# Performance work log

Hardware: AMD Instinct MI355X
Metric: run time of the kernel (lower is better)

Reference implementation:

```python
import jax, jax.numpy as jnp
import numpy as np

N = 100000
IN_DIM = 512
HID = 256
C = 64  # output_dim / num_classes
E = 1_600_000


def setup_inputs() -> dict:
    key = jax.random.key(0)
    ks = jax.random.split(key, 8)
    x = jax.random.normal(ks[0], (N, IN_DIM), dtype=jnp.float32)
    edge_index = jax.random.randint(ks[1], (2, E), 0, N, dtype=jnp.int64)
    # learned params (Linear stores W as [out,in]; we use [in,out] and matmul)
    W1 = jax.random.normal(ks[2], (IN_DIM, HID), dtype=jnp.float32) / np.sqrt(IN_DIM)
    b1 = jnp.zeros((HID,), dtype=jnp.float32)
    W2 = jax.random.normal(ks[3], (HID, C), dtype=jnp.float32) / np.sqrt(HID)
    b2 = jnp.zeros((C,), dtype=jnp.float32)
    Wp = jax.random.normal(ks[4], (C, 1), dtype=jnp.float32) / np.sqrt(C)
    bp = jnp.zeros((1,), dtype=jnp.float32)
    return {"x": x, "edge_index": edge_index, "K": 10,
            "W1": W1, "b1": b1, "W2": W2, "b2": b2, "Wp": Wp, "bp": bp}


def reference(x, edge_index, K, W1, b1, W2, b2, Wp, bp):
    n = x.shape[0]
    # MLP encoder (dropout is identity in eval mode)
    h = jax.nn.relu(x @ W1 + b1)
    h = h @ W2 + b2  # [N, C]

    # gcn_norm with add_remaining_self_loops (fill_value=1.0):
    # original self-loop edges are dropped (weight 0), fresh self loops appended.
    row, col = edge_index[0], edge_index[1]
    ew = jnp.where(row == col, 0.0, 1.0).astype(h.dtype)
    loops = jnp.arange(n, dtype=edge_index.dtype)
    row_f = jnp.concatenate([row, loops])
    col_f = jnp.concatenate([col, loops])
    ew_f = jnp.concatenate([ew, jnp.ones((n,), dtype=h.dtype)])
    deg = jax.ops.segment_sum(ew_f, col_f, num_segments=n)
    dinv = jnp.where(deg > 0, jax.lax.rsqrt(deg), 0.0)
    norm = dinv[row_f] * ew_f * dinv[col_f]  # [E+N]

    # K hops of normalized scatter-add propagation
    def hop(hc, _):
        m = jax.ops.segment_sum(norm[:, None] * hc[row_f], col_f, num_segments=n)
        return m, m

    _, hs = jax.lax.scan(hop, h, None, length=K)  # hs: [K, N, C]
    pps = jnp.concatenate([h[:, None, :], jnp.moveaxis(hs, 0, 1)], axis=1)  # [N, K+1, C]

    # learned per-hop retain scores + combine
    score = jax.nn.sigmoid((pps @ Wp + bp)[..., 0])  # [N, K+1]
    emb = jnp.einsum('nk,nkc->nc', score, pps)  # [N, C]
    return jax.nn.log_softmax(emb, axis=1), emb
```

## Files before the change

kernel.cpp:

```cpp
#include <hip/hip_runtime.h>
#include <hip/hip_fp16.h>

typedef unsigned short u16;
typedef short bf16x8 __attribute__((ext_vector_type(8)));
typedef float f32x4 __attribute__((ext_vector_type(4)));

#define IN_DIM 512
#define HID    256
#define C_DIM  64
#define KHOPS  10
#define CHUNK  2048

__device__ inline u16 f2bf(float v) {
    unsigned u = __float_as_uint(v);
    return (u16)((u + 0x7FFFu + ((u >> 16) & 1u)) >> 16);
}

__device__ inline void unpack8(uint4 u, float* f) {
    float2 a = __half22float2(*(__half2*)&u.x);
    float2 b = __half22float2(*(__half2*)&u.y);
    float2 c = __half22float2(*(__half2*)&u.z);
    float2 d = __half22float2(*(__half2*)&u.w);
    f[0] = a.x; f[1] = a.y; f[2] = b.x; f[3] = b.y;
    f[4] = c.x; f[5] = c.y; f[6] = d.x; f[7] = d.y;
}

__global__ void k_deg(const int* __restrict__ ei, int E, unsigned* __restrict__ deg) {
    int e = blockIdx.x * blockDim.x + threadIdx.x;
    if (e >= E) return;
    int r = ei[e], c = ei[E + e];
    if (r != c) atomicAdd(&deg[c], 1u);
}

__global__ void k_dinv(const unsigned* __restrict__ deg, float* __restrict__ dinv, int n) {
    int v = blockIdx.x * blockDim.x + threadIdx.x;
    if (v >= n) return;
    dinv[v] = 1.0f / sqrtf((float)(deg[v] + 1u));
}

__global__ __launch_bounds__(256) void k_scanA(const unsigned* __restrict__ cnt, int n,
                                               unsigned* __restrict__ bsum) {
    __shared__ unsigned sd[256];
    int base = blockIdx.x * CHUNK;
    unsigned s = 0;
    for (int i = threadIdx.x; i < CHUNK; i += 256) {
        int idx = base + i;
        s += (idx < n) ? cnt[idx] : 0u;
    }
    sd[threadIdx.x] = s;
    __syncthreads();
    for (int ofs = 128; ofs > 0; ofs >>= 1) {
        if (threadIdx.x < ofs) sd[threadIdx.x] += sd[threadIdx.x + ofs];
        __syncthreads();
    }
    if (threadIdx.x == 0) bsum[blockIdx.x] = sd[0];
}

__global__ void k_scanB(unsigned* bsum, int nch, unsigned* rowptrN) {
    if (threadIdx.x == 0 && blockIdx.x == 0) {
        unsigned run = 0;
        for (int i = 0; i < nch; i++) { unsigned t = bsum[i]; bsum[i] = run; run += t; }
        *rowptrN = run;
    }
}

__global__ __launch_bounds__(256) void k_scanC(const unsigned* __restrict__ cnt, int n,
                                               const unsigned* __restrict__ bsum,
                                               unsigned* __restrict__ rowptr) {
    __shared__ unsigned sd[256];
    const int PT = CHUNK / 256;
    int base = blockIdx.x * CHUNK;
    unsigned c[PT];
    unsigned tot = 0;
#pragma unroll
    for (int j = 0; j < PT; j++) {
        int idx = base + threadIdx.x * PT + j;
        c[j] = (idx < n) ? cnt[idx] : 0u;
        tot += c[j];
    }
    sd[threadIdx.x] = tot;
    __syncthreads();
    for (int ofs = 1; ofs < 256; ofs <<= 1) {
        unsigned vv = (threadIdx.x >= (unsigned)ofs) ? sd[threadIdx.x - ofs] : 0u;
        __syncthreads();
        sd[threadIdx.x] += vv;
        __syncthreads();
    }
    unsigned excl = sd[threadIdx.x] - tot;
    unsigned run = bsum[blockIdx.x] + excl;
#pragma unroll
    for (int j = 0; j < PT; j++) {
        int idx = base + threadIdx.x * PT + j;
        if (idx < n) rowptr[idx] = run;
        run += c[j];
    }
}

__global__ void k_fill(const int* __restrict__ ei, int E, const unsigned* __restrict__ rowptr,
                       unsigned* __restrict__ fill, const float* __restrict__ dinv,
                       int2* __restrict__ epack) {
    int e = blockIdx.x * blockDim.x + threadIdx.x;
    if (e >= E) return;
    int r = ei[e], c = ei[E + e];
    if (r == c) return;
    unsigned pos = rowptr[c] + atomicAdd(&fill[c], 1u);
    int2 p;
    p.x = r;
    p.y = __float_as_int(dinv[r] * dinv[c]);
    epack[pos] = p;
}

__global__ void k_prepw(const float* __restrict__ W, u16* __restrict__ T, int K, int N) {
    int t = blockIdx.x * blockDim.x + threadIdx.x;
    if (t >= K * N) return;
    int k = t / N, nn = t - k * N;
    T[(size_t)nn * K + k] = f2bf(W[t]);
}

__global__ __launch_bounds__(256) void k_gemm1_mfma(
    const float* __restrict__ X, const u16* __restrict__ BT,
    const float* __restrict__ b1, u16* __restrict__ C, int M) {
    __shared__ uint4 smem4[2048];
    u16* Ab = (u16*)smem4;
    u16* Bb = Ab + 8192;
    const int tid = threadIdx.x, l = tid & 63, w = tid >> 6;
    const int wr = w >> 1, wc = w & 1;
    const int row0 = blockIdx.x * 128, col0 = blockIdx.y * 128;
    const int srow = tid >> 1, skh = tid & 1;
    const int rsw = (srow >> 1) & 3;
    const int m15 = l & 15;
    const int slotoff = (((l >> 4) ^ ((l >> 1) & 3)) << 3);

    f32x4 acc[4][4];
#pragma unroll
    for (int i = 0; i < 4; i++)
#pragma unroll
        for (int j = 0; j < 4; j++) acc[i][j] = (f32x4){0.f, 0.f, 0.f, 0.f};

    float ax[16];
    uint4 rb[2];
    auto gload = [&](int t) {
        int k0 = t * 32;
        int grow = row0 + srow;
        if (grow < M) {
            const float* p = X + (size_t)grow * IN_DIM + k0 + skh * 16;
#pragma unroll
            for (int q = 0; q < 4; q++) *(float4*)&ax[q * 4] = *(const float4*)(p + q * 4);
        } else {
#pragma unroll
            for (int q = 0; q < 16; q++) ax[q] = 0.f;
        }
        const u16* pb = BT + (size_t)(col0 + srow) * IN_DIM + k0 + skh * 16;
        rb[0] = *(const uint4*)pb;
        rb[1] = *(const uint4*)(pb + 8);
    };
    auto lwrite = [&](int buf) {
#pragma unroll
        for (int g = 0; g < 2; g++) {
            unsigned wd[4];
#pragma unroll
            for (int q = 0; q < 4; q++)
                wd[q] = (unsigned)f2bf(ax[g * 8 + 2 * q]) | ((unsigned)f2bf(ax[g * 8 + 2 * q + 1]) << 16);
            uint4 H = {wd[0], wd[1], wd[2], wd[3]};
            int slot = (skh * 2 + g) ^ rsw;
            *(uint4*)&Ab[buf * 4096 + srow * 32 + (slot << 3)] = H;
            *(uint4*)&Bb[buf * 4096 + srow * 32 + (slot << 3)] = rb[g];
        }
    };

    gload(0);
    lwrite(0);
    __syncthreads();
    const int NT = IN_DIM / 32;
    for (int t = 0; t < NT; t++) {
        int buf = t & 1;
        if (t + 1 < NT) gload(t + 1);
        bf16x8 af[4], bf[4];
#pragma unroll
        for (int f = 0; f < 4; f++) {
            af[f] = *(bf16x8*)&Ab[buf * 4096 + (wr * 64 + f * 16 + m15) * 32 + slotoff];
            bf[f] = *(bf16x8*)&Bb[buf * 4096 + (wc * 64 + f * 16 + m15) * 32 + slotoff];
        }
#pragma unroll
        for (int i = 0; i < 4; i++)
#pragma unroll
            for (int j = 0; j < 4; j++)
                acc[i][j] = __builtin_amdgcn_mfma_f32_16x16x32_bf16(af[i], bf[j], acc[i][j], 0, 0, 0);
        if (t + 1 < NT) {
            __syncthreads();
            lwrite((t + 1) & 1);
            __syncthreads();
        }
    }
    __syncthreads();
    u16* ot = (u16*)smem4;
#pragma unroll
    for (int j = 0; j < 4; j++) {
        int col = col0 + wc * 64 + j * 16 + m15;
        float bb = b1[col];
        int coll = wc * 64 + j * 16 + m15;
#pragma unroll
        for (int i = 0; i < 4; i++)
#pragma unroll
            for (int r = 0; r < 4; r++) {
                int rowl = wr * 64 + i * 16 + (l >> 4) * 4 + r;
                ot[rowl * 128 + coll] = f2bf(fmaxf(acc[i][j][r] + bb, 0.f));
            }
    }
    __syncthreads();
#pragma unroll
    for (int p = 0; p < 8; p++) {
        int idx = p * 4096 + tid * 16;
        uint4 vv = *(uint4*)((char*)smem4 + idx);
        int row = p * 16 + (tid >> 4);
        int gcol = (tid & 15) * 8;
        int grow = row0 + row;
        if (grow < M) *(uint4*)(C + (size_t)grow * HID + col0 + gcol) = vv;
    }
}

__global__ __launch_bounds__(256) void k_gemm2_mfma(
    const u16* __restrict__ A1, const u16* __restrict__ BT,
    const float* __restrict__ b2, __half* __restrict__ H, int M) {
    __shared__ u16 Ab[2][128][32], Bb[2][64][32];
    const int tid = threadIdx.x, l = tid & 63, w = tid >> 6;
    const int wr = w >> 1, wc = w & 1;
    const int row0 = blockIdx.x * 128;
    const int srow = tid >> 1, skh = tid & 1;
    const int rsw = (srow >> 1) & 3;
    const int srow2 = tid >> 2, skq = tid & 3;
    const int rsw2 = (srow2 >> 1) & 3;
    const int m15 = l & 15;
    const int slotoff = (((l >> 4) ^ ((l >> 1) & 3)) << 3);

    f32x4 acc[4][2];
#pragma unroll
    for (int i = 0; i < 4; i++)
#pragma unroll
        for (int j = 0; j < 2; j++) acc[i][j] = (f32x4){0.f, 0.f, 0.f, 0.f};

    uint4 ra[2], rb2;
    auto gload = [&](int t) {
        int k0 = t * 32;
        int grow = row0 + srow;
        if (grow < M) {
            const u16* p = A1 + (size_t)grow * HID + k0 + skh * 16;
            ra[0] = *(const uint4*)p;
            ra[1] = *(const uint4*)(p + 8);
        } else {
            ra[0] = ra[1] = (uint4){0u, 0u, 0u, 0u};
        }
        rb2 = *(const uint4*)(BT + (size_t)srow2 * HID + k0 + skq * 8);
    };
    auto lwrite = [&](int buf) {
#pragma unroll
        for (int g = 0; g < 2; g++) {
            int slot = (skh * 2 + g) ^ rsw;
            *(uint4*)&Ab[buf][srow][slot << 3] = ra[g];
        }
        int slot2 = skq ^ rsw2;
        *(uint4*)&Bb[buf][srow2][slot2 << 3] = rb2;
    };

    gload(0);
    lwrite(0);
    __syncthreads();
    const int NT = HID / 32;
    for (int t = 0; t < NT; t++) {
        int buf = t & 1;
        if (t + 1 < NT) gload(t + 1);
        bf16x8 af[4], bf[2];
#pragma unroll
        for (int f = 0; f < 4; f++)
            af[f] = *(bf16x8*)&Ab[buf][wr * 64 + f * 16 + m15][slotoff];
#pragma unroll
        for (int f = 0; f < 2; f++)
            bf[f] = *(bf16x8*)&Bb[buf][wc * 32 + f * 16 + m15][slotoff];
#pragma unroll
        for (int i = 0; i < 4; i++)
#pragma unroll
            for (int j = 0; j < 2; j++)
                acc[i][j] = __builtin_amdgcn_mfma_f32_16x16x32_bf16(af[i], bf[j], acc[i][j], 0, 0, 0);
        if (t + 1 < NT) {
            __syncthreads();
            lwrite((t + 1) & 1);
            __syncthreads();
        }
    }
#pragma unroll
    for (int j = 0; j < 2; j++) {
        int col = wc * 32 + j * 16 + m15;
        float bb = b2[col];
#pragma unroll
        for (int i = 0; i < 4; i++)
#pragma unroll
            for (int r = 0; r < 4; r++) {
                int row = row0 + wr * 64 + i * 16 + (l >> 4) * 4 + r;
                if (row < M) H[(size_t)row * C_DIM + col] = __float2half(acc[i][j][r] + bb);
            }
    }
}

__global__ __launch_bounds__(256) void k_hop(
    const int* __restrict__ rowptr, const int2* __restrict__ epack,
    const float* __restrict__ dinv, const __half* __restrict__ hc, __half* __restrict__ hn,
    float* __restrict__ s_next, float* __restrict__ s_self,
    const float* __restrict__ Wp, int n) {
    const int lane = threadIdx.x & 63;
    const int wid = threadIdx.x >> 6;
    const int es = lane >> 3;
    const int ck = lane & 7;
    const int nw = gridDim.x * 4;
    float wp8[8];
#pragma unroll
    for (int q = 0; q < 8; q++) wp8[q] = Wp[ck * 8 + q];
    for (int v = blockIdx.x * 4 + wid; v < n; v += nw) {
        const int start = rowptr[v], end = rowptr[v + 1];
        const float di = dinv[v];
        uint4 hvu = *(const uint4*)(hc + (size_t)v * C_DIM + ck * 8);
        float hvf[8];
        unpack8(hvu, hvf);
        float acc[8];
#pragma unroll
        for (int q = 0; q < 8; q++) acc[q] = 0.f;
        int e = start + es;
        for (; e + 8 < end; e += 16) {
            int2 p0 = epack[e];
            int2 p1 = epack[e + 8];
            uint4 a0 = *(const uint4*)(hc + (size_t)p0.x * C_DIM + ck * 8);
            uint4 a1 = *(const uint4*)(hc + (size_t)p1.x * C_DIM + ck * 8);
            float w0 = __int_as_float(p0.y), w1 = __int_as_float(p1.y);
            float f0[8], f1[8];
            unpack8(a0, f0);
            unpack8(a1, f1);
#pragma unroll
            for (int q = 0; q < 8; q++) acc[q] = fmaf(w0, f0[q], acc[q]);
#pragma unroll
            for (int q = 0; q < 8; q++) acc[q] = fmaf(w1, f1[q], acc[q]);
        }
        if (e < end) {
            int2 p = epack[e];
            uint4 a = *(const uint4*)(hc + (size_t)p.x * C_DIM + ck * 8);
            float w = __int_as_float(p.y);
            float f[8];
            unpack8(a, f);
#pragma unroll
            for (int q = 0; q < 8; q++) acc[q] = fmaf(w, f[q], acc[q]);
        }
#pragma unroll
        for (int m = 8; m < 64; m <<= 1)
#pragma unroll
            for (int q = 0; q < 8; q++) acc[q] += __shfl_xor(acc[q], m, 64);
        const float dd = di * di;
#pragma unroll
        for (int q = 0; q < 8; q++) acc[q] = fmaf(dd, hvf[q], acc[q]);
        if (es == 0) {
            __half2 o0 = __floats2half2_rn(acc[0], acc[1]);
            __half2 o1 = __floats2half2_rn(acc[2], acc[3]);
            __half2 o2 = __floats2half2_rn(acc[4], acc[5]);
            __half2 o3 = __floats2half2_rn(acc[6], acc[7]);
            uint4 o;
            o.x = *(unsigned*)&o0; o.y = *(unsigned*)&o1;
            o.z = *(unsigned*)&o2; o.w = *(unsigned*)&o3;
            *(uint4*)(hn + (size_t)v * C_DIM + ck * 8) = o;
        }
        float pr = 0.f;
#pragma unroll
        for (int q = 0; q < 8; q++) pr = fmaf(acc[q], wp8[q], pr);
#pragma unroll
        for (int m = 1; m < 8; m <<= 1) pr += __shfl_xor(pr, m, 64);
        if (lane == 0) s_next[v] = pr;
        if (s_self) {
            float p0 = 0.f;
#pragma unroll
            for (int q = 0; q < 8; q++) p0 = fmaf(hvf[q], wp8[q], p0);
#pragma unroll
            for (int m = 1; m < 8; m <<= 1) p0 += __shfl_xor(p0, m, 64);
            if (lane == 0) s_self[v] = p0;
        }
    }
}

__global__ __launch_bounds__(256) void k_out(
    const __half* __restrict__ hkall, const float* __restrict__ scores,
    const float* __restrict__ bp, float* __restrict__ out, int n) {
    const int lane = threadIdx.x & 63;
    const int wid = threadIdx.x >> 6;
    const int nw = gridDim.x * 4;
    const float bps = bp[0];
    const size_t stride = (size_t)n * C_DIM;
    for (int v = blockIdx.x * 4 + wid; v < n; v += nw) {
        float embv = 0.f;
        const __half* hp = hkall + (size_t)v * C_DIM + lane;
#pragma unroll
        for (int k = 0; k < KHOPS + 1; k++) {
            float pk = scores[(size_t)k * n + v];
            float s = 1.f / (1.f + expf(-(pk + bps)));
            embv = fmaf(s, __half2float(hp[(size_t)k * stride]), embv);
        }
        float mx = embv;
#pragma unroll
        for (int m = 32; m > 0; m >>= 1) mx = fmaxf(mx, __shfl_xor(mx, m, 64));
        float ex = expf(embv - mx);
        float sm = ex;
#pragma unroll
        for (int m = 32; m > 0; m >>= 1) sm += __shfl_xor(sm, m, 64);
        float ls = embv - mx - logf(sm);
        out[(size_t)v * C_DIM + lane] = ls;
        out[(size_t)n * C_DIM + (size_t)v * C_DIM + lane] = embv;
    }
}

extern "C" void kernel_launch(void* const* d_in, const int* in_sizes, int n_in,
                              void* d_out, int out_size, void* d_ws, size_t ws_size,
                              hipStream_t stream) {
    const float* x  = (const float*)d_in[0];
    const int*   ei = (const int*)d_in[1];
    const float* W1 = (const float*)d_in[3];
    const float* b1 = (const float*)d_in[4];
    const float* W2 = (const float*)d_in[5];
    const float* b2 = (const float*)d_in[6];
    const float* Wp = (const float*)d_in[7];
    const float* bp = (const float*)d_in[8];
    const int n = in_sizes[0] / IN_DIM;
    const int E = in_sizes[1] / 2;
    float* out = (float*)d_out;

    char* ws = (char*)d_ws;
    size_t off = 0;
    auto alloc = [&](size_t bytes) { void* p = ws + off; off += (bytes + 511) & ~511ULL; return p; };
    unsigned* deg    = (unsigned*)alloc((size_t)n * 4);
    unsigned* fill   = (unsigned*)alloc((size_t)n * 4);
    unsigned* rowptr = (unsigned*)alloc((size_t)(n + 1) * 4);
    unsigned* bsum   = (unsigned*)alloc(1024 * 4);
    float* dinv      = (float*)alloc((size_t)n * 4);
    int2* epack      = (int2*)alloc((size_t)E * 8);
    u16* W1T         = (u16*)alloc((size_t)IN_DIM * HID * 2);
    u16* W2T         = (u16*)alloc((size_t)HID * C_DIM * 2);
    const size_t hkelems = (size_t)n * C_DIM;
    __half* hkall    = (__half*)alloc((size_t)(KHOPS + 1) * hkelems * 2);
    u16* h1          = (u16*)(hkall + hkelems);
    float* scores    = (float*)alloc((size_t)(KHOPS + 1) * n * 4);

    hipMemsetAsync(deg, 0, (size_t)n * 4, stream);
    hipMemsetAsync(fill, 0, (size_t)n * 4, stream);

    const int tb = 256;
    k_deg<<<(E + tb - 1) / tb, tb, 0, stream>>>(ei, E, deg);
    k_dinv<<<(n + tb - 1) / tb, tb, 0, stream>>>(deg, dinv, n);
    int nch = (n + CHUNK - 1) / CHUNK;
    k_scanA<<<nch, 256, 0, stream>>>(deg, n, bsum);
    k_scanB<<<1, 64, 0, stream>>>(bsum, nch, rowptr + n);
    k_scanC<<<nch, 256, 0, stream>>>(deg, n, bsum, rowptr);
    k_fill<<<(E + tb - 1) / tb, tb, 0, stream>>>(ei, E, rowptr, fill, dinv, epack);

    k_prepw<<<(IN_DIM * HID + tb - 1) / tb, tb, 0, stream>>>(W1, W1T, IN_DIM, HID);
    k_prepw<<<(HID * C_DIM + tb - 1) / tb, tb, 0, stream>>>(W2, W2T, HID, C_DIM);

    k_gemm1_mfma<<<dim3((n + 127) / 128, 2), 256, 0, stream>>>(x, W1T, b1, h1, n);
    k_gemm2_mfma<<<(n + 127) / 128, 256, 0, stream>>>(h1, W2T, b2, hkall, n);

    int hop_blocks = (n + 3) / 4;
    if (hop_blocks > 2048) hop_blocks = 2048;
    for (int k = 0; k < KHOPS; k++) {
        k_hop<<<hop_blocks, 256, 0, stream>>>(
            (const int*)rowptr, epack, dinv, hkall + (size_t)k * hkelems,
            hkall + (size_t)(k + 1) * hkelems,
            scores + (size_t)(k + 1) * n, (k == 0) ? scores : (float*)nullptr, Wp, n);
    }
    k_out<<<hop_blocks, 256, 0, stream>>>(hkall, scores, bp, out, n);
}
```

Measured before the change: 793.5 us.

## Double-register prefetch in GEMM1 and drop redundant barriers in both GEMMs

The first GEMM loop is restructured to keep two register staging sets (A and B) and unroll by two. Global loads for tile t+2 or t+3 are issued while tile t is computed, and each K step now needs only one barrier instead of two. The second GEMM drops the barrier before its shared-memory write, relying on the previous iteration's trailing barrier to make the target buffer free. This trades extra registers, which may affect occupancy, for deeper latency hiding and less synchronisation in a stage that is a small part of total runtime.

Measured after the change: 805.9 us. About the same (+1.6%).

```diff
diff --git a/kernel.cpp b/kernel.cpp
--- a/kernel.cpp
+++ b/kernel.cpp
@@ -137,44 +137,66 @@
 #pragma unroll
         for (int j = 0; j < 4; j++) acc[i][j] = (f32x4){0.f, 0.f, 0.f, 0.f};
 
-    float ax[16];
-    uint4 rb[2];
-    auto gload = [&](int t) {
+    float axA[16], axB[16];
+    uint4 rbA[2], rbB[2];
+    const int grow = row0 + srow;
+    const float* xrow = X + (size_t)grow * IN_DIM + skh * 16;
+    const u16* brow = BT + (size_t)(col0 + srow) * IN_DIM + skh * 16;
+    const bool rowok = grow < M;
+
+    auto gloadA = [&](int t) {
         int k0 = t * 32;
-        int grow = row0 + srow;
-        if (grow < M) {
-            const float* p = X + (size_t)grow * IN_DIM + k0 + skh * 16;
-#pragma unroll
-            for (int q = 0; q < 4; q++) *(float4*)&ax[q * 4] = *(const float4*)(p + q * 4);
+        if (rowok) {
+#pragma unroll
+            for (int q = 0; q < 4; q++) *(float4*)&axA[q * 4] = *(const float4*)(xrow + k0 + q * 4);
         } else {
 #pragma unroll
-            for (int q = 0; q < 16; q++) ax[q] = 0.f;
-        }
-        const u16* pb = BT + (size_t)(col0 + srow) * IN_DIM + k0 + skh * 16;
-        rb[0] = *(const uint4*)pb;
-        rb[1] = *(const uint4*)(pb + 8);
-    };
-    auto lwrite = [&](int buf) {
+            for (int q = 0; q < 16; q++) axA[q] = 0.f;
+        }
+        rbA[0] = *(const uint4*)(brow + k0);
+        rbA[1] = *(const uint4*)(brow + k0 + 8);
+    };
+    auto gloadB = [&](int t) {
+        int k0 = t * 32;
+        if (rowok) {
+#pragma unroll
+            for (int q = 0; q < 4; q++) *(float4*)&axB[q * 4] = *(const float4*)(xrow + k0 + q * 4);
+        } else {
+#pragma unroll
+            for (int q = 0; q < 16; q++) axB[q] = 0.f;
+        }
+        rbB[0] = *(const uint4*)(brow + k0);
+        rbB[1] = *(const uint4*)(brow + k0 + 8);
+    };
+    auto lwriteA = [&](int buf) {
 #pragma unroll
         for (int g = 0; g < 2; g++) {
             unsigned wd[4];
 #pragma unroll
             for (int q = 0; q < 4; q++)
-                wd[q] = (unsigned)f2bf(ax[g * 8 + 2 * q]) | ((unsigned)f2bf(ax[g * 8 + 2 * q + 1]) << 16);
+                wd[q] = (unsigned)f2bf(axA[g * 8 + 2 * q]) |
+                        ((unsigned)f2bf(axA[g * 8 + 2 * q + 1]) << 16);
             uint4 H = {wd[0], wd[1], wd[2], wd[3]};
             int slot = (skh * 2 + g) ^ rsw;
             *(uint4*)&Ab[buf * 4096 + srow * 32 + (slot << 3)] = H;
-            *(uint4*)&Bb[buf * 4096 + srow * 32 + (slot << 3)] = rb[g];
-        }
-    };
-
-    gload(0);
-    lwrite(0);
-    __syncthreads();
-    const int NT = IN_DIM / 32;
-    for (int t = 0; t < NT; t++) {
-        int buf = t & 1;
-        if (t + 1 < NT) gload(t + 1);
+            *(uint4*)&Bb[buf * 4096 + srow * 32 + (slot << 3)] = rbA[g];
+        }
+    };
+    auto lwriteB = [&](int buf) {
+#pragma unroll
+        for (int g = 0; g < 2; g++) {
+            unsigned wd[4];
+#pragma unroll
+            for (int q = 0; q < 4; q++)
+                wd[q] = (unsigned)f2bf(axB[g * 8 + 2 * q]) |
+                        ((unsigned)f2bf(axB[g * 8 + 2 * q + 1]) << 16);
+            uint4 H = {wd[0], wd[1], wd[2], wd[3]};
+            int slot = (skh * 2 + g) ^ rsw;
+            *(uint4*)&Ab[buf * 4096 + srow * 32 + (slot << 3)] = H;
+            *(uint4*)&Bb[buf * 4096 + srow * 32 + (slot << 3)] = rbB[g];
+        }
+    };
+    auto docompute = [&](int buf) {
         bf16x8 af[4], bf[4];
 #pragma unroll
         for (int f = 0; f < 4; f++) {
@@ -186,10 +208,27 @@
 #pragma unroll
             for (int j = 0; j < 4; j++)
                 acc[i][j] = __builtin_amdgcn_mfma_f32_16x16x32_bf16(af[i], bf[j], acc[i][j], 0, 0, 0);
+    };
+
+    const int NT = IN_DIM / 32;
+    gloadA(0);
+    lwriteA(0);
+    gloadB(1);
+    __syncthreads();
+    for (int t = 0; t < NT; t += 2) {
+        docompute(0);
+        if (t + 2 < NT) gloadA(t + 2);
         if (t + 1 < NT) {
+            lwriteB(1);
             __syncthreads();
-            lwrite((t + 1) & 1);
-            __syncthreads();
+        }
+        if (t + 1 < NT) {
+            docompute(1);
+            if (t + 3 < NT) gloadB(t + 3);
+            if (t + 2 < NT) {
+                lwriteA(0);
+                __syncthreads();
+            }
         }
     }
     __syncthreads();
@@ -214,8 +253,8 @@
         uint4 vv = *(uint4*)((char*)smem4 + idx);
         int row = p * 16 + (tid >> 4);
         int gcol = (tid & 15) * 8;
-        int grow = row0 + row;
-        if (grow < M) *(uint4*)(C + (size_t)grow * HID + col0 + gcol) = vv;
+        int growo = row0 + row;
+        if (growo < M) *(uint4*)(C + (size_t)growo * HID + col0 + gcol) = vv;
     }
 }
 
@@ -282,7 +321,6 @@
             for (int j = 0; j < 2; j++)
                 acc[i][j] = __builtin_amdgcn_mfma_f32_16x16x32_bf16(af[i], bf[j], acc[i][j], 0, 0, 0);
         if (t + 1 < NT) {
-            __syncthreads();
             lwrite((t + 1) & 1);
             __syncthreads();
         }
```
